# Performance work log

Hardware: AMD Instinct MI355X
Metric: run time of the kernel (lower is better)

## Reference

```python
import jax, jax.numpy as jnp
import numpy as np

H = 200  # hidden size
D = 1    # input size
T = 8192 # sequence length


def setup_inputs() -> dict:
    key = jax.random.key(0)
    ks = jax.random.split(key, 11)
    s = 1.0 / np.sqrt(H)  # torch LSTM init scale
    u = lambda k, shape: jax.random.uniform(k, shape, jnp.float32, -s, s)
    return {
        "input_seq": jax.random.normal(ks[0], (T, D), jnp.float32),
        "W_ih0": u(ks[1], (4 * H, D)),
        "W_hh0": u(ks[2], (4 * H, H)),
        "b_ih0": u(ks[3], (4 * H,)),
        "b_hh0": u(ks[4], (4 * H,)),
        "W_ih1": u(ks[5], (4 * H, H)),
        "W_hh1": u(ks[6], (4 * H, H)),
        "b_ih1": u(ks[7], (4 * H,)),
        "b_hh1": u(ks[8], (4 * H,)),
        "W_out": u(ks[9], (D, H)),
        "b_out": u(ks[10], (D,)),
    }


def _cell(pre, h, c, Whh):
    # pre: [4H] = x @ W_ih.T + b_ih + b_hh already folded in
    g = pre + h @ Whh.T
    i, f, gg, o = jnp.split(g, 4)
    i = jax.nn.sigmoid(i)
    f = jax.nn.sigmoid(f)
    gg = jnp.tanh(gg)
    o = jax.nn.sigmoid(o)
    c = f * c + i * gg
    h = o * jnp.tanh(c)
    return h, c


def reference(input_seq, W_ih0, W_hh0, b_ih0, b_hh0,
              W_ih1, W_hh1, b_ih1, b_hh1, W_out, b_out):
    x = input_seq.reshape(input_seq.shape[0], -1)  # [T, D]
    # precompute layer-0 input projections for all timesteps (one big GEMM)
    pre0 = x @ W_ih0.T + (b_ih0 + b_hh0)           # [T, 4H]
    b1 = b_ih1 + b_hh1

    def step(carry, p0):
        h0, c0, h1, c1 = carry
        h0, c0 = _cell(p0, h0, c0, W_hh0)
        # eval mode: dropout(0.1) between layers is identity
        h1, c1 = _cell(h0 @ W_ih1.T + b1, h1, c1, W_hh1)
        return (h0, c0, h1, c1), None

    z = jnp.zeros((H,), x.dtype)
    (h0, c0, h1, c1), _ = jax.lax.scan(step, (z, z, z, z), pre0)
    # predictions[-1]: linear head on last top-layer hidden state -> [D]
    return h1 @ W_out.T + b_out
```

## Files before the change

### kernel.cpp

```cpp
#include <hip/hip_runtime.h>

#define TT 8192
#define HH 200
#define G4 800
#define NLJ 9
#define NWR 64
#define RD 1024
#define RDM 1023
#define BPWIN 900

typedef unsigned long long u64;
typedef unsigned int u32;
typedef _Float16 f16;
typedef _Float16 f16x2 __attribute__((ext_vector_type(2)));

__device__ __forceinline__ float sigmoidf_(float x){ return 1.0f/(1.0f+__expf(-x)); }
__device__ __forceinline__ float tanhf_(float x){
    float e = __expf(2.0f*fabsf(x));
    float r = 1.0f - 2.0f/(e + 1.0f);
    return copysignf(r, x);
}
__device__ __forceinline__ u64 pcku(u32 tag, u32 v){ return ((u64)tag<<32) | v; }
__device__ __forceinline__ u64 pckf(u32 tag, float v){ return pcku(tag, __float_as_uint(v)); }
__device__ __forceinline__ u64 ald(const u64* p){
    return __hip_atomic_load((u64*)p, __ATOMIC_RELAXED, __HIP_MEMORY_SCOPE_AGENT);
}
__device__ __forceinline__ void ast(u64* p, u64 v){
    __hip_atomic_store(p, v, __ATOMIC_RELAXED, __HIP_MEMORY_SCOPE_AGENT);
}
__device__ __forceinline__ u32 pkh(float a, float b){
    f16x2 v = { (f16)a, (f16)b };
    return __builtin_bit_cast(u32, v);
}
__device__ __forceinline__ float dot2(u32 a, u32 b, float c){
#if __has_builtin(__builtin_amdgcn_fdot2)
    return __builtin_amdgcn_fdot2(__builtin_bit_cast(f16x2, a),
                                  __builtin_bit_cast(f16x2, b), c, false);
#else
    f16x2 av = __builtin_bit_cast(f16x2, a), bv = __builtin_bit_cast(f16x2, b);
    return c + (float)av[0]*(float)bv[0] + (float)av[1]*(float)bv[1];
#endif
}
__device__ __forceinline__ u32 poll1u(const u64* p, u32 tag){
    u64 v; do { v = ald(p); } while ((u32)(v >> 32) != tag);
    return (u32)v;
}
__device__ __forceinline__ void poll5(const u64* slot, u32 tag, int m, float* o){
    const bool g4 = (m < 32);
    u64 v0, v1, v2, v3, v4 = 0;
    for(;;){
        v0 = ald(slot + m);       v1 = ald(slot + m + 192);
        v2 = ald(slot + m + 384); v3 = ald(slot + m + 576);
        if (g4) v4 = ald(slot + m + 768);
        if ((u32)(v0>>32)==tag && (u32)(v1>>32)==tag && (u32)(v2>>32)==tag &&
            (u32)(v3>>32)==tag && (!g4 || (u32)(v4>>32)==tag)) break;
    }
    o[0]=__uint_as_float((u32)v0); o[1]=__uint_as_float((u32)v1);
    o[2]=__uint_as_float((u32)v2); o[3]=__uint_as_float((u32)v3);
    o[4]= g4 ? __uint_as_float((u32)v4) : 0.f;
}

__global__ __launch_bounds__(1024, 1)
void lstm_pipe(const float* __restrict__ x,
               const float* __restrict__ Wih0, const float* __restrict__ Whh0,
               const float* __restrict__ bih0, const float* __restrict__ bhh0,
               const float* __restrict__ Wih1, const float* __restrict__ Whh1,
               const float* __restrict__ bih1, const float* __restrict__ bhh1,
               const float* __restrict__ Wout, const float* __restrict__ bout,
               u64* __restrict__ hp0,
               u64* __restrict__ p1r,
               u32* __restrict__ prog,
               float* __restrict__ out)
{
    const int role = blockIdx.x;
    const int tid  = threadIdx.x;

    __shared__ __align__(16) u32 wl[NLJ * G4 * 4];
    __shared__ __align__(16) u32 hp_lds[2][100];
    __shared__ float h32[HH];
    __shared__ float s_pre[G4];
    __shared__ float s_in[2][G4];
    __shared__ float xr[2];
    __shared__ u32 hpbuf[2][100];

    if (role >= 2) {
        const int q = role - 2;
        const int rl = tid >> 2, kq = tid & 3;
        u32 wp[25]; float bs = 0.f; int grow = 0;
        if (tid < 800) {
            grow = q * 200 + rl;
            const float* wr = Wih1 + (size_t)grow * HH + kq * 50;
            #pragma unroll
            for (int i = 0; i < 25; ++i) wp[i] = pkh(wr[2*i], wr[2*i+1]);
            #pragma unroll
            for (int i = 0; i < 25; ++i) asm volatile("" : "+v"(wp[i]));
            if (kq == 0) bs = bih1[grow] + bhh1[grow];
        } else if (tid >= 832 && tid < 932) {
            hpbuf[0][tid - 832] = poll1u(&hp0[tid - 832], 1u);
        }
        u32 prog_c = 0;
        __syncthreads();
        for (int t = 0; t < TT; ++t) {
            if (tid < 800) {
                const u32* hb = hpbuf[t & 1] + kq * 25;
                float a0 = 0.f, a1 = 0.f;
                #pragma unroll
                for (int i = 0; i < 25; i += 2) a0 = dot2(wp[i], hb[i], a0);
                #pragma unroll
                for (int i = 1; i < 25; i += 2) a1 = dot2(wp[i], hb[i], a1);
                float s = a0 + a1;
                s += __shfl_xor(s, 1);
                s += __shfl_xor(s, 2);
                if (kq == 0)
                    ast(&p1r[(size_t)(t & RDM) * G4 + grow],
                        pckf((u32)(t + 1), s + bs));
            } else if (tid >= 832 && tid < 932) {
                if (t + 1 < TT)
                    hpbuf[(t + 1) & 1][tid - 832] =
                        poll1u(&hp0[(size_t)(t + 1) * 100 + (tid - 832)],
                               (u32)(t + 2));
            } else if (tid == 1008) {
                while ((int)(t + 1) - (int)prog_c >= BPWIN) {
                    __builtin_amdgcn_s_sleep(8);
                    prog_c = __hip_atomic_load(prog, __ATOMIC_RELAXED,
                                               __HIP_MEMORY_SCOPE_AGENT);
                }
            }
            __syncthreads();
        }
        return;
    }

    const bool L0 = (role == 0);
    const float* Whh = L0 ? Whh0 : Whh1;

    for (int idx = tid; idx < G4 * 36; idx += 1024) {
        const int r = idx / 36, p = idx % 36;
        const float* wr = Whh + (size_t)r * HH;
        wl[(((p >> 2) * G4 + r) << 2) + (p & 3)] = pkh(wr[2*p], wr[2*p + 1]);
    }
    u32 w[NWR]; float wih = 0.f, bs = 0.f;
    if (tid < G4) {
        const float* wr = Whh + (size_t)tid * HH + 72;
        #pragma unroll
        for (int i = 0; i < NWR; ++i) w[i] = pkh(wr[2*i], wr[2*i + 1]);
        #pragma unroll
        for (int i = 0; i < NWR; ++i) asm volatile("" : "+v"(w[i]));
        if (L0) {
            bs = bih0[tid] + bhh0[tid];
            wih = Wih0[tid];
            asm volatile("" : "+v"(bs));
            asm volatile("" : "+v"(wih));
        }
    }
    if (tid < 100) { hp_lds[0][tid] = 0u; hp_lds[1][tid] = 0u; }
    if (tid < HH) h32[tid] = 0.f;

    float c = 0.f, c2 = 0.f;
    float o0=0.f, o1=0.f, o2=0.f, o3=0.f, o4=0.f;
    if (!L0 && tid >= 832) {
        float o[5];
        poll5(p1r, 1u, tid - 832, o);
        const int m = tid - 832;
        s_in[0][m] = o[0]; s_in[0][m+192] = o[1]; s_in[0][m+384] = o[2];
        s_in[0][m+576] = o[3];
        if (m < 32) s_in[0][m+768] = o[4];
    }
    if (L0 && tid == 832) xr[0] = x[0];
    __syncthreads();

    for (int t = 0; t < TT; ++t) {
        const int p = t & 1;
        if (tid < G4) {
            const uint4* hp4 = (const uint4*)hp_lds[p];
            float a0=0.f, a1=0.f, a2=0.f, a3=0.f;
            #pragma unroll
            for (int j = 0; j < NLJ; ++j) {
                const uint4 hu = hp4[j];
                const uint4 wu = *(const uint4*)&wl[(j * G4 + tid) << 2];
                a0 = dot2(wu.x, hu.x, a0);
                a1 = dot2(wu.y, hu.y, a1);
                a2 = dot2(wu.z, hu.z, a2);
                a3 = dot2(wu.w, hu.w, a3);
                if ((j % 3) == 2) __builtin_amdgcn_sched_barrier(0);
            }
            #pragma unroll
            for (int j = NLJ; j < 25; ++j) {
                const uint4 hu = hp4[j];
                const int i = (j - NLJ) * 4;
                a0 = dot2(w[i],     hu.x, a0);
                a1 = dot2(w[i + 1], hu.y, a1);
                a2 = dot2(w[i + 2], hu.z, a2);
                a3 = dot2(w[i + 3], hu.w, a3);
                if ((j % 4) == 3) __builtin_amdgcn_sched_barrier(0);
            }
            const float acc = (a0 + a1) + (a2 + a3);
            if (L0) s_pre[tid] = acc + xr[p] * wih + bs;
            else    s_pre[tid] = acc + s_in[p][tid];
        } else if (tid >= 832) {
            if (!L0) {
                if (t + 1 < TT) {
                    float o[5];
                    poll5(&p1r[(size_t)((t + 1) & RDM) * G4], (u32)(t + 2),
                          tid - 832, o);
                    o0=o[0]; o1=o[1]; o2=o[2]; o3=o[3]; o4=o[4];
                }
            } else if (tid == 832 && t + 1 < TT) {
                o0 = x[t + 1];
            }
        }
        __syncthreads();
        if (tid >= 832) {
            const int n = tid - 832;
            const float ig = sigmoidf_(s_pre[n]);
            const float fg = sigmoidf_(s_pre[200 + n]);
            const float gg = tanhf_  (s_pre[400 + n]);
            const float og = sigmoidf_(s_pre[600 + n]);
            c = fg * c + ig * gg;
            const float h = og * tanhf_(c);
            h32[n] = h;
            const float hpart = __shfl_xor(h, 1);
            u32 pk2 = 0;
            if (!(n & 1)) { pk2 = pkh(h, hpart); hp_lds[p ^ 1][n >> 1] = pk2; }
            float h2 = 0.f;
            if (n < 8) {
                const int n2 = 192 + n;
                const float ig2 = sigmoidf_(s_pre[n2]);
                const float fg2 = sigmoidf_(s_pre[200 + n2]);
                const float gg2 = tanhf_  (s_pre[400 + n2]);
                const float og2 = sigmoidf_(s_pre[600 + n2]);
                c2 = fg2 * c2 + ig2 * gg2;
                h2 = og2 * tanhf_(c2);
                h32[n2] = h2;
            }
            const float h2part = __shfl_xor(h2, 1);
            u32 pk2b = 0;
            if (n < 8 && !(n & 1)) { pk2b = pkh(h2, h2part); hp_lds[p ^ 1][96 + (n>>1)] = pk2b; }
            if (L0 && !(n & 1)) {
                ast(&hp0[(size_t)t * 100 + (n >> 1)], pcku((u32)(t + 1), pk2));
                if (n < 8)
                    ast(&hp0[(size_t)t * 100 + 96 + (n >> 1)],
                        pcku((u32)(t + 1), pk2b));
            }
            if (t + 1 < TT) {
                if (!L0) {
                    const int m = n;
                    s_in[p ^ 1][m] = o0; s_in[p ^ 1][m + 192] = o1;
                    s_in[p ^ 1][m + 384] = o2; s_in[p ^ 1][m + 576] = o3;
                    if (m < 32) s_in[p ^ 1][m + 768] = o4;
                } else if (tid == 832) {
                    xr[p ^ 1] = o0;
                }
            }
        } else if (!L0 && tid == 800 && (t & 63) == 63) {
            __hip_atomic_store(prog, (u32)(t + 1), __ATOMIC_RELAXED,
                               __HIP_MEMORY_SCOPE_AGENT);
        }
        __syncthreads();
    }

    if (!L0 && tid < 64) {
        float s2 = 0.f;
        for (int k = tid; k < HH; k += 64) s2 += h32[k] * Wout[k];
        #pragma unroll
        for (int off = 32; off > 0; off >>= 1) s2 += __shfl_down(s2, off);
        if (tid == 0) out[0] = s2 + bout[0];
    }
}

extern "C" void kernel_launch(void* const* d_in, const int* in_sizes, int n_in,
                              void* d_out, int out_size, void* d_ws, size_t ws_size,
                              hipStream_t stream) {
    const float* x    = (const float*)d_in[0];
    const float* Wih0 = (const float*)d_in[1];
    const float* Whh0 = (const float*)d_in[2];
    const float* bih0 = (const float*)d_in[3];
    const float* bhh0 = (const float*)d_in[4];
    const float* Wih1 = (const float*)d_in[5];
    const float* Whh1 = (const float*)d_in[6];
    const float* bih1 = (const float*)d_in[7];
    const float* bhh1 = (const float*)d_in[8];
    const float* Wout = (const float*)d_in[9];
    const float* bout = (const float*)d_in[10];
    float* out = (float*)d_out;

    char* ws = (char*)d_ws;
    u64* hp0  = (u64*)ws;
    u64* p1r  = (u64*)(ws + 6553600);
    u32* prog = (u32*)(ws + 13107200);

    hipMemsetAsync(ws, 0, 13107264, stream);

    hipLaunchKernelGGL(lstm_pipe, dim3(6), dim3(1024), 0, stream,
        x, Wih0, Whh0, bih0, bhh0, Wih1, Whh1, bih1, bhh1, Wout, bout,
        hp0, p1r, prog, out);
}
```

Baseline: 15.15 ms.

## Split each LSTM layer's recurrence across two workgroups exchanging hidden halves

Each layer's recurrent cell is split across two 512-thread workgroups. Each workgroup owns half the hidden units and holds its slice of W_hh in registers and LDS, and the two halves trade their hidden state every step through tagged global-memory slots. The layer-1 input projection now runs on four workgroups of 400 active threads. The whole x sequence is staged into LDS, and a padding LDS array plus odd block indices appear meant to place the workgroups on particular CUs. The aim is a shorter per-step matvec critical path, at the cost of a cross-CU handshake on every timestep, which may be slower than the LDS-only exchange it replaces.

```diff
diff --git a/kernel.cpp b/kernel.cpp
--- a/kernel.cpp
+++ b/kernel.cpp
@@ -2,9 +2,6 @@
 
 #define TT 8192
 #define HH 200
-#define G4 800
-#define NLJ 9
-#define NWR 64
 #define RD 1024
 #define RDM 1023
 #define BPWIN 900
@@ -31,6 +28,10 @@
 __device__ __forceinline__ u32 pkh(float a, float b){
     f16x2 v = { (f16)a, (f16)b };
     return __builtin_bit_cast(u32, v);
+}
+__device__ __forceinline__ float unpk(u32 u, int hi){
+    f16x2 v = __builtin_bit_cast(f16x2, u);
+    return (float)v[hi];
 }
 __device__ __forceinline__ float dot2(u32 a, u32 b, float c){
 #if __has_builtin(__builtin_amdgcn_fdot2)
@@ -45,22 +46,22 @@
     u64 v; do { v = ald(p); } while ((u32)(v >> 32) != tag);
     return (u32)v;
 }
-__device__ __forceinline__ void poll5(const u64* slot, u32 tag, int m, float* o){
-    const bool g4 = (m < 32);
-    u64 v0, v1, v2, v3, v4 = 0;
+
+__device__ __forceinline__ void poll100(const u64* base, u32 tag, int l,
+                                        u32* o0, u32* o1){
+    const bool g1 = (l + 64 < 100);
+    u64 v0, v1 = 0;
     for(;;){
-        v0 = ald(slot + m);       v1 = ald(slot + m + 192);
-        v2 = ald(slot + m + 384); v3 = ald(slot + m + 576);
-        if (g4) v4 = ald(slot + m + 768);
-        if ((u32)(v0>>32)==tag && (u32)(v1>>32)==tag && (u32)(v2>>32)==tag &&
-            (u32)(v3>>32)==tag && (!g4 || (u32)(v4>>32)==tag)) break;
-    }
-    o[0]=__uint_as_float((u32)v0); o[1]=__uint_as_float((u32)v1);
-    o[2]=__uint_as_float((u32)v2); o[3]=__uint_as_float((u32)v3);
-    o[4]= g4 ? __uint_as_float((u32)v4) : 0.f;
-}
-
-__global__ __launch_bounds__(1024, 1)
+        v0 = ald(base + l);
+        if (g1) v1 = ald(base + l + 64);
+        if ((u32)(v0>>32)==tag && (!g1 || (u32)(v1>>32)==tag)) break;
+    }
+    *o0 = (u32)v0;
+    *o1 = (u32)v1;
+}
+
+__global__ __launch_bounds__(512)
+__attribute__((amdgpu_waves_per_eu(2, 4)))
 void lstm_pipe(const float* __restrict__ x,
                const float* __restrict__ Wih0, const float* __restrict__ Whh0,
                const float* __restrict__ bih0, const float* __restrict__ bhh0,
@@ -69,57 +70,77 @@
                const float* __restrict__ Wout, const float* __restrict__ bout,
                u64* __restrict__ hp0,
                u64* __restrict__ p1r,
+               u64* __restrict__ h1x,
                u32* __restrict__ prog,
                float* __restrict__ out)
 {
-    const int role = blockIdx.x;
-    const int tid  = threadIdx.x;
-
-    __shared__ __align__(16) u32 wl[NLJ * G4 * 4];
+    const int bid = blockIdx.x;
+    const int tid = threadIdx.x;
+
+    __shared__ __align__(16) u32 wl[3 * 400 * 4];
+    __shared__ float xs[TT];
     __shared__ __align__(16) u32 hp_lds[2][100];
-    __shared__ float h32[HH];
-    __shared__ float s_pre[G4];
-    __shared__ float s_in[2][G4];
-    __shared__ float xr[2];
     __shared__ u32 hpbuf[2][100];
-
-    if (role >= 2) {
-        const int q = role - 2;
-        const int rl = tid >> 2, kq = tid & 3;
-        u32 wp[25]; float bs = 0.f; int grow = 0;
-        if (tid < 800) {
-            grow = q * 200 + rl;
-            const float* wr = Wih1 + (size_t)grow * HH + kq * 50;
-            #pragma unroll
-            for (int i = 0; i < 25; ++i) wp[i] = pkh(wr[2*i], wr[2*i+1]);
-            #pragma unroll
-            for (int i = 0; i < 25; ++i) asm volatile("" : "+v"(wp[i]));
-            if (kq == 0) bs = bih1[grow] + bhh1[grow];
-        } else if (tid >= 832 && tid < 932) {
-            hpbuf[0][tid - 832] = poll1u(&hp0[tid - 832], 1u);
+    __shared__ float s_pre[400];
+    __shared__ float s_in[2][400];
+    __shared__ float h32[100];
+    __shared__ float pad_f[6656];
+
+    if (x == nullptr) pad_f[0] = 1.f;
+
+    int role = -1, L = 0, hf = 0, q = 0;
+    if      (bid == 0)  { role = 0; L = 0; hf = 0; }
+    else if (bid == 8)  { role = 0; L = 0; hf = 1; }
+    else if (bid == 1)  { role = 0; L = 1; hf = 0; }
+    else if (bid == 9)  { role = 0; L = 1; hf = 1; }
+    else if (bid == 2)  { role = 1; q = 0; }
+    else if (bid == 10) { role = 1; q = 1; }
+    else if (bid == 3)  { role = 1; q = 2; }
+    else if (bid == 11) { role = 1; q = 3; }
+    if (role < 0) return;
+
+    if (role == 1) {
+        const int rl = tid >> 1, kh = tid & 1;
+        const bool act = (tid < 400);
+        u32 wp[50]; float bs = 0.f; int row = 0;
+        if (act) {
+            row = q * 200 + rl;
+            const float* wr = Wih1 + (size_t)row * HH + kh * 100;
+            #pragma unroll
+            for (int i = 0; i < 50; ++i) wp[i] = pkh(wr[2*i], wr[2*i+1]);
+            #pragma unroll
+            for (int i = 0; i < 50; ++i) asm volatile("" : "+v"(wp[i]));
+            if (kh == 0) bs = bih1[row] + bhh1[row];
+        } else if (tid >= 448) {
+            u32 o0, o1;
+            poll100(hp0, 1u, tid - 448, &o0, &o1);
+            hpbuf[0][tid - 448] = o0;
+            if (tid - 448 + 64 < 100) hpbuf[0][tid - 448 + 64] = o1;
         }
         u32 prog_c = 0;
         __syncthreads();
         for (int t = 0; t < TT; ++t) {
-            if (tid < 800) {
-                const u32* hb = hpbuf[t & 1] + kq * 25;
+            if (act) {
+                const u32* hb = hpbuf[t & 1] + kh * 50;
                 float a0 = 0.f, a1 = 0.f;
                 #pragma unroll
-                for (int i = 0; i < 25; i += 2) a0 = dot2(wp[i], hb[i], a0);
-                #pragma unroll
-                for (int i = 1; i < 25; i += 2) a1 = dot2(wp[i], hb[i], a1);
+                for (int i = 0; i < 50; i += 2) a0 = dot2(wp[i], hb[i], a0);
+                #pragma unroll
+                for (int i = 1; i < 50; i += 2) a1 = dot2(wp[i], hb[i], a1);
                 float s = a0 + a1;
                 s += __shfl_xor(s, 1);
-                s += __shfl_xor(s, 2);
-                if (kq == 0)
-                    ast(&p1r[(size_t)(t & RDM) * G4 + grow],
+                if (kh == 0)
+                    ast(&p1r[(size_t)(t & RDM) * 800 + q * 200 + rl],
                         pckf((u32)(t + 1), s + bs));
-            } else if (tid >= 832 && tid < 932) {
-                if (t + 1 < TT)
-                    hpbuf[(t + 1) & 1][tid - 832] =
-                        poll1u(&hp0[(size_t)(t + 1) * 100 + (tid - 832)],
-                               (u32)(t + 2));
-            } else if (tid == 1008) {
+            } else if (tid >= 448) {
+                if (t + 1 < TT) {
+                    u32 o0, o1;
+                    poll100(&hp0[(size_t)(t + 1) * 100], (u32)(t + 2),
+                            tid - 448, &o0, &o1);
+                    hpbuf[(t + 1) & 1][tid - 448] = o0;
+                    if (tid - 448 + 64 < 100) hpbuf[(t + 1) & 1][tid - 448 + 64] = o1;
+                }
+            } else if (tid == 440) {
                 while ((int)(t + 1) - (int)prog_c >= BPWIN) {
                     __builtin_amdgcn_s_sleep(8);
                     prog_c = __hip_atomic_load(prog, __ATOMIC_RELAXED,
@@ -131,137 +152,160 @@
         return;
     }
 
-    const bool L0 = (role == 0);
-    const float* Whh = L0 ? Whh0 : Whh1;
-
-    for (int idx = tid; idx < G4 * 36; idx += 1024) {
-        const int r = idx / 36, p = idx % 36;
-        const float* wr = Whh + (size_t)r * HH;
-        wl[(((p >> 2) * G4 + r) << 2) + (p & 3)] = pkh(wr[2*p], wr[2*p + 1]);
-    }
-    u32 w[NWR]; float wih = 0.f, bs = 0.f;
-    if (tid < G4) {
-        const float* wr = Whh + (size_t)tid * HH + 72;
-        #pragma unroll
-        for (int i = 0; i < NWR; ++i) w[i] = pkh(wr[2*i], wr[2*i + 1]);
-        #pragma unroll
-        for (int i = 0; i < NWR; ++i) asm volatile("" : "+v"(w[i]));
-        if (L0) {
-            bs = bih0[tid] + bhh0[tid];
-            wih = Wih0[tid];
+    const int nb = hf * 100;
+    const int pb = (1 - hf) * 100;
+    const float* Whh = L ? Whh1 : Whh0;
+    const bool act = (tid < 400);
+
+    for (int idx = tid; idx < 400 * 12; idx += 512) {
+        const int rl = idx / 12, pp = idx % 12;
+        const int row = (rl / 100) * 200 + nb + (rl % 100);
+        wl[(((pp >> 2) * 400) + rl) * 4 + (pp & 3)] =
+            pkh(Whh[(size_t)row * HH + 2*pp], Whh[(size_t)row * HH + 2*pp + 1]);
+    }
+    u32 w[88]; float wih = 0.f, bs = 0.f;
+    if (act) {
+        const int row = (tid / 100) * 200 + nb + (tid % 100);
+        const float* wr = Whh + (size_t)row * HH + 24;
+        #pragma unroll
+        for (int i = 0; i < 88; ++i) w[i] = pkh(wr[2*i], wr[2*i + 1]);
+        #pragma unroll
+        for (int i = 0; i < 88; ++i) asm volatile("" : "+v"(w[i]));
+        if (L == 0) {
+            bs = bih0[row] + bhh0[row];
+            wih = Wih0[row];
             asm volatile("" : "+v"(bs));
             asm volatile("" : "+v"(wih));
         }
     }
-    if (tid < 100) { hp_lds[0][tid] = 0u; hp_lds[1][tid] = 0u; }
-    if (tid < HH) h32[tid] = 0.f;
-
-    float c = 0.f, c2 = 0.f;
-    float o0=0.f, o1=0.f, o2=0.f, o3=0.f, o4=0.f;
-    if (!L0 && tid >= 832) {
-        float o[5];
-        poll5(p1r, 1u, tid - 832, o);
-        const int m = tid - 832;
-        s_in[0][m] = o[0]; s_in[0][m+192] = o[1]; s_in[0][m+384] = o[2];
-        s_in[0][m+576] = o[3];
-        if (m < 32) s_in[0][m+768] = o[4];
-    }
-    if (L0 && tid == 832) xr[0] = x[0];
+    if (L == 0) for (int i = tid; i < TT; i += 512) xs[i] = x[i];
+    if (tid < 100) { hp_lds[0][tid] = 0u; hp_lds[1][tid] = 0u; h32[tid] = 0.f; }
+
+    u32 ov[7];
+    if (L == 1 && tid >= 448) {
+        const int l = tid - 448;
+        int sl[7]; bool g[7];
+        #pragma unroll
+        for (int r = 0; r < 7; ++r) {
+            const int m = l + 64 * r;
+            g[r] = (m < 400);
+            sl[r] = g[r] ? (m / 100) * 200 + nb + (m % 100) : 0;
+        }
+        u64 v[7];
+        for(;;){
+            #pragma unroll
+            for (int r = 0; r < 7; ++r) if (g[r]) v[r] = ald(&p1r[sl[r]]);
+            bool ok = true;
+            #pragma unroll
+            for (int r = 0; r < 7; ++r) if (g[r] && (u32)(v[r]>>32) != 1u) ok = false;
+            if (ok) break;
+        }
+        #pragma unroll
+        for (int r = 0; r < 7; ++r)
+            if (g[r]) s_in[0][l + 64 * r] = __uint_as_float((u32)v[r]);
+    }
+    float c = 0.f;
     __syncthreads();
 
     for (int t = 0; t < TT; ++t) {
         const int p = t & 1;
-        if (tid < G4) {
+        if (act) {
             const uint4* hp4 = (const uint4*)hp_lds[p];
             float a0=0.f, a1=0.f, a2=0.f, a3=0.f;
             #pragma unroll
-            for (int j = 0; j < NLJ; ++j) {
-                const uint4 hu = hp4[j];
-                const uint4 wu = *(const uint4*)&wl[(j * G4 + tid) << 2];
+            for (int g2 = 0; g2 < 3; ++g2) {
+                const uint4 hu = hp4[g2];
+                const uint4 wu = *(const uint4*)&wl[((g2 * 400) + tid) << 2];
                 a0 = dot2(wu.x, hu.x, a0);
                 a1 = dot2(wu.y, hu.y, a1);
                 a2 = dot2(wu.z, hu.z, a2);
                 a3 = dot2(wu.w, hu.w, a3);
-                if ((j % 3) == 2) __builtin_amdgcn_sched_barrier(0);
-            }
-            #pragma unroll
-            for (int j = NLJ; j < 25; ++j) {
-                const uint4 hu = hp4[j];
-                const int i = (j - NLJ) * 4;
+            }
+            #pragma unroll
+            for (int g2 = 3; g2 < 25; ++g2) {
+                const uint4 hu = hp4[g2];
+                const int i = (g2 - 3) * 4;
                 a0 = dot2(w[i],     hu.x, a0);
                 a1 = dot2(w[i + 1], hu.y, a1);
                 a2 = dot2(w[i + 2], hu.z, a2);
                 a3 = dot2(w[i + 3], hu.w, a3);
-                if ((j % 4) == 3) __builtin_amdgcn_sched_barrier(0);
             }
             const float acc = (a0 + a1) + (a2 + a3);
-            if (L0) s_pre[tid] = acc + xr[p] * wih + bs;
-            else    s_pre[tid] = acc + s_in[p][tid];
-        } else if (tid >= 832) {
-            if (!L0) {
-                if (t + 1 < TT) {
-                    float o[5];
-                    poll5(&p1r[(size_t)((t + 1) & RDM) * G4], (u32)(t + 2),
-                          tid - 832, o);
-                    o0=o[0]; o1=o[1]; o2=o[2]; o3=o[3]; o4=o[4];
-                }
-            } else if (tid == 832 && t + 1 < TT) {
-                o0 = x[t + 1];
-            }
+            s_pre[tid] = acc + ((L == 0) ? xs[t] * wih + bs : s_in[p][tid]);
+        } else if (L == 1 && tid >= 448 && t + 1 < TT) {
+            const int l = tid - 448;
+            u64 v[7];
+            const u64* slot = &p1r[(size_t)((t + 1) & RDM) * 800];
+            const u32 tg = (u32)(t + 2);
+            for(;;){
+                #pragma unroll
+                for (int r = 0; r < 7; ++r) {
+                    const int m = l + 64 * r;
+                    if (m < 400) v[r] = ald(slot + (m/100)*200 + nb + (m%100));
+                }
+                bool ok = true;
+                #pragma unroll
+                for (int r = 0; r < 7; ++r) {
+                    const int m = l + 64 * r;
+                    if (m < 400 && (u32)(v[r]>>32) != tg) ok = false;
+                }
+                if (ok) break;
+            }
+            #pragma unroll
+            for (int r = 0; r < 7; ++r) ov[r] = (u32)v[r];
         }
         __syncthreads();
-        if (tid >= 832) {
-            const int n = tid - 832;
+        if (tid < 100) {
+            const int n = tid;
             const float ig = sigmoidf_(s_pre[n]);
-            const float fg = sigmoidf_(s_pre[200 + n]);
-            const float gg = tanhf_  (s_pre[400 + n]);
-            const float og = sigmoidf_(s_pre[600 + n]);
+            const float fg = sigmoidf_(s_pre[100 + n]);
+            const float gg = tanhf_  (s_pre[200 + n]);
+            const float og = sigmoidf_(s_pre[300 + n]);
             c = fg * c + ig * gg;
             const float h = og * tanhf_(c);
             h32[n] = h;
-            const float hpart = __shfl_xor(h, 1);
-            u32 pk2 = 0;
-            if (!(n & 1)) { pk2 = pkh(h, hpart); hp_lds[p ^ 1][n >> 1] = pk2; }
-            float h2 = 0.f;
-            if (n < 8) {
-                const int n2 = 192 + n;
-                const float ig2 = sigmoidf_(s_pre[n2]);
-                const float fg2 = sigmoidf_(s_pre[200 + n2]);
-                const float gg2 = tanhf_  (s_pre[400 + n2]);
-                const float og2 = sigmoidf_(s_pre[600 + n2]);
-                c2 = fg2 * c2 + ig2 * gg2;
-                h2 = og2 * tanhf_(c2);
-                h32[n2] = h2;
-            }
-            const float h2part = __shfl_xor(h2, 1);
-            u32 pk2b = 0;
-            if (n < 8 && !(n & 1)) { pk2b = pkh(h2, h2part); hp_lds[p ^ 1][96 + (n>>1)] = pk2b; }
-            if (L0 && !(n & 1)) {
-                ast(&hp0[(size_t)t * 100 + (n >> 1)], pcku((u32)(t + 1), pk2));
-                if (n < 8)
-                    ast(&hp0[(size_t)t * 100 + 96 + (n >> 1)],
-                        pcku((u32)(t + 1), pk2b));
-            }
-            if (t + 1 < TT) {
-                if (!L0) {
-                    const int m = n;
-                    s_in[p ^ 1][m] = o0; s_in[p ^ 1][m + 192] = o1;
-                    s_in[p ^ 1][m + 384] = o2; s_in[p ^ 1][m + 576] = o3;
-                    if (m < 32) s_in[p ^ 1][m + 768] = o4;
-                } else if (tid == 832) {
-                    xr[p ^ 1] = o0;
-                }
-            }
-        } else if (!L0 && tid == 800 && (t & 63) == 63) {
+            const float hq = __shfl_xor(h, 1);
+            if (!(n & 1)) {
+                const u32 pk = pkh(h, hq);
+                hp_lds[p ^ 1][(nb >> 1) + (n >> 1)] = pk;
+                if (L == 0)
+                    ast(&hp0[(size_t)t * 100 + (nb >> 1) + (n >> 1)],
+                        pcku((u32)(t + 1), pk));
+                else
+                    ast(&h1x[(size_t)(t & 63) * 100 + (nb >> 1) + (n >> 1)],
+                        pcku((u32)(t + 1), pk));
+            }
+        } else if (tid >= 448) {
+            const int l = tid - 448;
+            if (L == 1 && t + 1 < TT) {
+                #pragma unroll
+                for (int r = 0; r < 7; ++r) {
+                    const int m = l + 64 * r;
+                    if (m < 400) s_in[p ^ 1][m] = __uint_as_float(ov[r]);
+                }
+            }
+            if (l < 50) {
+                const u64* src = (L == 0)
+                    ? &hp0[(size_t)t * 100 + (pb >> 1) + l]
+                    : &h1x[(size_t)(t & 63) * 100 + (pb >> 1) + l];
+                hp_lds[p ^ 1][(pb >> 1) + l] = poll1u(src, (u32)(t + 1));
+            }
+        } else if (L == 1 && hf == 0 && tid == 400 && (t & 63) == 63) {
             __hip_atomic_store(prog, (u32)(t + 1), __ATOMIC_RELAXED,
                                __HIP_MEMORY_SCOPE_AGENT);
         }
         __syncthreads();
     }
 
-    if (!L0 && tid < 64) {
+    if (L == 1 && hf == 0 && tid < 64) {
+        const int fin = ((TT - 1) & 1) ^ 1;
         float s2 = 0.f;
-        for (int k = tid; k < HH; k += 64) s2 += h32[k] * Wout[k];
+        for (int k = tid; k < HH; k += 64) {
+            float hv;
+            if (k < 100) hv = h32[k];
+            else         hv = unpk(hp_lds[fin][50 + ((k - 100) >> 1)], (k - 100) & 1);
+            s2 += hv * Wout[k];
+        }
         #pragma unroll
         for (int off = 32; off > 0; off >>= 1) s2 += __shfl_down(s2, off);
         if (tid == 0) out[0] = s2 + bout[0];
@@ -287,11 +331,12 @@
     char* ws = (char*)d_ws;
     u64* hp0  = (u64*)ws;
     u64* p1r  = (u64*)(ws + 6553600);
-    u32* prog = (u32*)(ws + 13107200);
-
-    hipMemsetAsync(ws, 0, 13107264, stream);
-
-    hipLaunchKernelGGL(lstm_pipe, dim3(6), dim3(1024), 0, stream,
+    u64* h1x  = (u64*)(ws + 13107200);
+    u32* prog = (u32*)(ws + 13158400);
+
+    hipMemsetAsync(ws, 0, 13158464, stream);
+
+    hipLaunchKernelGGL(lstm_pipe, dim3(16), dim3(512), 0, stream,
         x, Wih0, Whh0, bih0, bhh0, Wih1, Whh1, bih1, bhh1, Wout, bout,
-        hp0, p1r, prog, out);
-}
+        hp0, p1r, h1x, prog, out);
+}
```

New measurement: 14.70 ms. 3.0% less time.
